# Optimization experiments

Measured on AMD Instinct MI355X. Metric: run time of the kernel, lower is better.

Reference implementation:

```python
import jax, jax.numpy as jnp
import numpy as np

N, E, IN, H, D, M, HID = 20000, 640000, 256, 8, 16, 3, 128


def setup_inputs() -> dict:
    key = jax.random.key(0)
    ks = jax.random.split(key, 9)
    h = jax.random.normal(ks[0], (N, IN), jnp.float32)
    # scale params for numerically sane attention logits
    fc_W = jax.random.normal(ks[1], (M, IN, H * D), jnp.float32) / np.sqrt(IN).astype(np.float32)
    attn_l = jax.random.normal(ks[2], (M, H, D), jnp.float32) * 0.1
    attn_r = jax.random.normal(ks[3], (M, H, D), jnp.float32) * 0.1
    bias = jnp.zeros((M, H * D), jnp.float32)
    edge_w = jax.random.uniform(ks[4], (M, E), jnp.float32)
    src = jax.random.randint(ks[5], (M, E), 0, N, jnp.int32)
    dst = jax.random.randint(ks[6], (M, E), 0, N, jnp.int32)
    sem_W1 = jax.random.normal(ks[7], (H * D, HID), jnp.float32) / np.sqrt(H * D).astype(np.float32)
    sem_b1 = jnp.zeros((HID,), jnp.float32)
    sem_w2 = jax.random.normal(ks[8], (HID,), jnp.float32) / np.sqrt(HID).astype(np.float32)
    return dict(h=h, fc_W=fc_W, attn_l=attn_l, attn_r=attn_r, bias=bias,
                edge_w=edge_w, sem_W1=sem_W1, sem_b1=sem_b1, sem_w2=sem_w2,
                src=src, dst=dst)


def _gat(h, W, al, ar, b, ew, s, d):
    # AdvGATConv forward, eval mode (dropout identity), residual=False
    ft = (h @ W).reshape(N, H, D)                      # [N,H,D]
    el = (ft * al).sum(-1)                             # [N,H]
    er = (ft * ar).sum(-1)                             # [N,H]
    # edge scores: (el_u + er_v) * edge_weight, then LeakyReLU(0.2)
    e = jax.nn.leaky_relu((el[s] + er[d]) * ew[:, None], 0.2)  # [E,H]
    # edge_softmax: segment softmax over incoming edges per dst node
    mx = jax.ops.segment_max(e, d, num_segments=N)
    mx = jnp.where(jnp.isfinite(mx), mx, 0.0)          # empty segments -> 0
    ex = jnp.exp(e - jax.lax.stop_gradient(mx)[d])
    denom = jax.ops.segment_sum(ex, d, num_segments=N)
    a = ex / denom[d]                                  # [E,H]
    # u_mul_e + sum: gather src feats, weight, scatter-add to dst
    out = jax.ops.segment_sum(ft[s] * a[:, :, None], d, num_segments=N)
    out = out + b.reshape(1, H, D)
    return jax.nn.elu(out).reshape(N, H * D)


def reference(h, fc_W, attn_l, attn_r, bias, edge_w, sem_W1, sem_b1, sem_w2, src, dst):
    embs = [_gat(h, fc_W[i], attn_l[i], attn_r[i], bias[i], edge_w[i], src[i], dst[i])
            for i in range(M)]
    z = jnp.stack(embs, axis=1)                        # [N, M, H*D]
    # SemanticAttention: mean over nodes of w2 . tanh(z W1 + b1), softmax over M
    w = (jnp.tanh(z @ sem_W1 + sem_b1) @ sem_w2).mean(0)  # [M]
    beta = jax.nn.softmax(w)
    return jnp.einsum('nmf,m->nf', z, beta)            # [N, H*D]
```

## Files before the change

### kernel.cpp

```cpp
#include <hip/hip_runtime.h>
#include <math.h>

#define NN 20000
#define NE 640000
#define NIN 256
#define NH 8
#define HD 16
#define NM 3
#define NF 128
#define HID 128
#define NSEG (NM * NN)
#define CAP 128

typedef __attribute__((ext_vector_type(4))) _Float16 half4;
typedef __attribute__((ext_vector_type(8))) _Float16 half8;
typedef __attribute__((ext_vector_type(4))) float f32x4;

__device__ __forceinline__ void atomAddF(float* p, float v) {
  unsafeAtomicAdd(p, v);
}

__global__ void k_prep(const float* __restrict__ h, const float* __restrict__ fcW,
                       const float* __restrict__ W1, _Float16* __restrict__ h16,
                       _Float16* __restrict__ WT, _Float16* __restrict__ W1T,
                       int* __restrict__ cursor, float* __restrict__ wsum) {
  int t = blockIdx.x * 256 + threadIdx.x;
  if (t < NN * NIN / 4) {
    float4 v = *(const float4*)(h + 4 * t);
    half4 o = {(_Float16)v.x, (_Float16)v.y, (_Float16)v.z, (_Float16)v.w};
    *(half4*)(h16 + 4 * t) = o;
  }
  if (t < NM * NIN * NF) {
    int mm = t >> 15;
    int n = (t >> 8) & 127;
    int k = t & 255;
    WT[t] = (_Float16)fcW[(mm << 15) + (k << 7) + n];
  }
  if (t < NF * HID) {
    int n = t >> 7;
    int k = t & 127;
    W1T[t] = (_Float16)W1[k * HID + n];
  }
  if (t < NSEG) cursor[t] = 0;
  if (t < 8) wsum[t] = 0.0f;
}

__device__ __forceinline__ void fill_body(int fb, const int* __restrict__ src,
                                          const int* __restrict__ dst,
                                          const float* __restrict__ ew,
                                          int* __restrict__ cursor,
                                          unsigned* __restrict__ erec) {
  int e4 = (fb * 256 + threadIdx.x) * 4;
  if (e4 >= NM * NE) return;
  int4 d4 = *(const int4*)(dst + e4);
  int4 s4 = *(const int4*)(src + e4);
  float4 w4 = *(const float4*)(ew + e4);
  const int dd[4] = {d4.x, d4.y, d4.z, d4.w};
  const int ss[4] = {s4.x, s4.y, s4.z, s4.w};
  const float ww[4] = {w4.x, w4.y, w4.z, w4.w};
  int seg[4], pos[4];
#pragma unroll
  for (int j = 0; j < 4; ++j) {
    int m = (e4 + j) / NE;
    seg[j] = m * NN + dd[j];
    pos[j] = atomicAdd(cursor + seg[j], 1);
  }
#pragma unroll
  for (int j = 0; j < 4; ++j) {
    unsigned wq = (unsigned)fminf(ww[j] * 131072.f, 131071.f);
    if (pos[j] < CAP)
      __builtin_nontemporal_store(((unsigned)ss[j] << 17) | wq,
                                  erec + (size_t)seg[j] * CAP + pos[j]);
  }
}

__device__ __forceinline__ void gemm_body(int g, const _Float16* __restrict__ h16,
                                          const _Float16* __restrict__ WT,
                                          const float* __restrict__ al,
                                          const float* __restrict__ ar,
                                          _Float16* __restrict__ fth,
                                          float* __restrict__ el,
                                          float* __restrict__ er) {
  int bx = g % 313, by = g / 313;
  int tid = threadIdx.x;
  int wave = tid >> 6, lane = tid & 63;
  int l15 = lane & 15, kslot = lane >> 4;
  int m = by >> 1;
  int cin = (by & 1) << 6;
  int rowbase = bx * 64 + wave * 16;
  int arow = rowbase + l15;
  bool aok = arow < NN;
  const _Float16* Ap = h16 + (size_t)(aok ? arow : 0) * NIN + kslot * 8;
  const _Float16* Bp = WT + ((size_t)m * NF + cin + l15) * NIN + kslot * 8;
  f32x4 acc[4];
#pragma unroll
  for (int c = 0; c < 4; ++c) acc[c] = (f32x4){0.f, 0.f, 0.f, 0.f};
#pragma unroll
  for (int kk = 0; kk < 8; ++kk) {
    int k0 = kk * 32;
    half8 a = {};
    if (aok) a = *(const half8*)(Ap + k0);
#pragma unroll
    for (int c = 0; c < 4; ++c) {
      half8 b = *(const half8*)(Bp + (size_t)c * 16 * NIN + k0);
      acc[c] = __builtin_amdgcn_mfma_f32_16x16x32_f16(a, b, acc[c], 0, 0, 0);
    }
  }
  int orow0 = rowbase + kslot * 4;
#pragma unroll
  for (int j = 0; j < 4; ++j) {
    int r = orow0 + j;
    if (r < NN) {
      _Float16* op = fth + ((size_t)m * NN + r) * NF + cin + l15;
#pragma unroll
      for (int c = 0; c < 4; ++c) op[c * 16] = (_Float16)acc[c][j];
    }
  }
  float alr[4], arr_[4];
#pragma unroll
  for (int c = 0; c < 4; ++c) {
    int head = (cin >> 4) + c;
    alr[c] = al[(m * NH + head) * HD + l15];
    arr_[c] = ar[(m * NH + head) * HD + l15];
  }
#pragma unroll
  for (int c = 0; c < 4; ++c) {
    int head = (cin >> 4) + c;
#pragma unroll
    for (int j = 0; j < 4; ++j) {
      float v = acc[c][j] * alr[c];
      float u = acc[c][j] * arr_[c];
#pragma unroll
      for (int off = 1; off < 16; off <<= 1) {
        v += __shfl_xor(v, off);
        u += __shfl_xor(u, off);
      }
      int r = orow0 + j;
      if (l15 == 0 && r < NN) {
        size_t idx = ((size_t)m * NN + r) * NH + head;
        el[idx] = v;
        er[idx] = u;
      }
    }
  }
}

__global__ __launch_bounds__(256) void k_fill_gemm(
    const int* __restrict__ src, const int* __restrict__ dst,
    const float* __restrict__ ew, int* __restrict__ cursor,
    unsigned* __restrict__ erec, const _Float16* __restrict__ h16,
    const _Float16* __restrict__ WT, const float* __restrict__ al,
    const float* __restrict__ ar, _Float16* __restrict__ fth,
    float* __restrict__ el, float* __restrict__ er) {
  int idx = blockIdx.x;
  int half_ = idx >> 1;
  if (idx & 1) {
    if (half_ < 1878) gemm_body(half_, h16, WT, al, ar, fth, el, er);
  } else {
    if (half_ < 1875) fill_body(half_, src, dst, ew, cursor, erec);
  }
}

__global__ __launch_bounds__(256) void k_aggr8(
    const int* __restrict__ cursor, const unsigned* __restrict__ erec,
    const float* __restrict__ el, const float* __restrict__ er,
    const _Float16* __restrict__ fth, const float* __restrict__ bias,
    _Float16* __restrict__ zh) {
  int wid = (blockIdx.x * 256 + threadIdx.x) >> 6;
  int lane = threadIdx.x & 63;
  if (wid >= NSEG) return;
  int m = wid / NN;
  int cnt = cursor[wid];
  cnt = cnt < CAP ? cnt : CAP;
  const unsigned* rp = erec + (size_t)wid * CAP;
  int g = lane >> 3, l8 = lane & 7;
  int h2 = l8;
  int c0 = l8 * 16;
  float er2 = er[wid * NH + h2];
  const float* elm = el + (size_t)m * NN * NH;
  const _Float16* fhm = fth + (size_t)m * NN * NF;

  float mx = -1e30f, sm = 0.f;
  float acc[16] = {};
  for (int i = g; i < cnt; i += 8) {
    unsigned rec = rp[i];
    int s = rec >> 17;
    float w = ((rec & 131071u) + 0.5f) * (1.f / 131072.f);
    float x = (elm[s * NH + h2] + er2) * w;
    x = x > 0.f ? x : 0.2f * x;
    float nmx = fmaxf(mx, x);
    float f = __expf(mx - nmx);
    float e = __expf(x - nmx);
    mx = nmx;
    sm = sm * f + e;
    const _Float16* fp = fhm + (size_t)s * NF + c0;
    half8 q0 = *(const half8*)(fp);
    half8 q1 = *(const half8*)(fp + 8);
#pragma unroll
    for (int k = 0; k < 8; ++k) acc[k] = fmaf(e, (float)q0[k], acc[k] * f);
#pragma unroll
    for (int k = 0; k < 8; ++k) acc[8 + k] = fmaf(e, (float)q1[k], acc[8 + k] * f);
  }
#pragma unroll
  for (int d = 8; d <= 32; d <<= 1) {
    float omx = __shfl_xor(mx, d);
    float osm = __shfl_xor(sm, d);
    float nmx = fmaxf(mx, omx);
    float f1 = __expf(mx - nmx), f2 = __expf(omx - nmx);
    sm = sm * f1 + osm * f2;
#pragma unroll
    for (int k = 0; k < 16; ++k) {
      float o = __shfl_xor(acc[k], d);
      acc[k] = acc[k] * f1 + o * f2;
    }
    mx = nmx;
  }
  if (g == 0) {
    float inv = sm > 0.f ? 1.f / sm : 0.f;
    const float* bp = bias + m * NF + c0;
    half8 zo0, zo1;
#pragma unroll
    for (int k = 0; k < 8; ++k) {
      float q = fmaf(acc[k], inv, bp[k]);
      q = q > 0.f ? q : __expf(q) - 1.f;
      zo0[k] = (_Float16)q;
      float q2 = fmaf(acc[8 + k], inv, bp[8 + k]);
      q2 = q2 > 0.f ? q2 : __expf(q2) - 1.f;
      zo1[k] = (_Float16)q2;
    }
    *(half8*)(zh + (size_t)wid * NF + c0) = zo0;
    *(half8*)(zh + (size_t)wid * NF + c0 + 8) = zo1;
  }
}

__global__ __launch_bounds__(256) void k_semgemm_mfma(
    const _Float16* __restrict__ zh, const _Float16* __restrict__ W1T,
    const float* __restrict__ b1, const float* __restrict__ w2,
    float* __restrict__ wsum) {
  __shared__ float msum[NM];
  int tid = threadIdx.x;
  if (tid < NM) msum[tid] = 0.f;
  __syncthreads();
  int wave = tid >> 6, lane = tid & 63;
  int l15 = lane & 15, kslot = lane >> 4;
  int rowbase = blockIdx.x * 64 + wave * 16;
  int arow = rowbase + l15;
  bool aok = arow < NSEG;
  const _Float16* Ap = zh + (size_t)(aok ? arow : 0) * NF + kslot * 8;
  const _Float16* Bp = W1T + (size_t)l15 * HID + kslot * 8;
  f32x4 acc[8];
#pragma unroll
  for (int c = 0; c < 8; ++c) acc[c] = (f32x4){0.f, 0.f, 0.f, 0.f};
#pragma unroll
  for (int kk = 0; kk < 4; ++kk) {
    int k0 = kk * 32;
    half8 a = {};
    if (aok) a = *(const half8*)(Ap + k0);
#pragma unroll
    for (int c = 0; c < 8; ++c) {
      half8 b = *(const half8*)(Bp + (size_t)c * 16 * HID + k0);
      acc[c] = __builtin_amdgcn_mfma_f32_16x16x32_f16(a, b, acc[c], 0, 0, 0);
    }
  }
  float p[4] = {0.f, 0.f, 0.f, 0.f};
#pragma unroll
  for (int c = 0; c < 8; ++c) {
    int col = c * 16 + l15;
    float b1r = b1[col];
    float w2r = w2[col];
#pragma unroll
    for (int j = 0; j < 4; ++j) p[j] += w2r * tanhf(acc[c][j] + b1r);
  }
#pragma unroll
  for (int j = 0; j < 4; ++j) {
#pragma unroll
    for (int off = 1; off < 16; off <<= 1) p[j] += __shfl_xor(p[j], off);
  }
  if (l15 == 0) {
#pragma unroll
    for (int j = 0; j < 4; ++j) {
      int r = rowbase + kslot * 4 + j;
      if (r < NSEG) atomicAdd(&msum[r / NN], p[j]);
    }
  }
  __syncthreads();
  if (tid < NM) {
    float v = msum[tid];
    if (v != 0.f) atomAddF(wsum + tid, v);
  }
}

__global__ void k_out8(const _Float16* __restrict__ zh, const float* __restrict__ wsum,
                       float* __restrict__ out) {
  int t = blockIdx.x * 256 + threadIdx.x;
  if (t >= NN * NF / 8) return;
  float w0 = wsum[0] * (1.f / NN);
  float w1 = wsum[1] * (1.f / NN);
  float w2v = wsum[2] * (1.f / NN);
  float mxw = fmaxf(w0, fmaxf(w1, w2v));
  float e0 = __expf(w0 - mxw), e1 = __expf(w1 - mxw), e2 = __expf(w2v - mxw);
  float inv = 1.f / (e0 + e1 + e2);
  e0 *= inv; e1 *= inv; e2 *= inv;
  size_t base = (size_t)t * 8;
  half8 z0 = *(const half8*)(zh + base);
  half8 z1 = *(const half8*)(zh + (size_t)NN * NF + base);
  half8 z2 = *(const half8*)(zh + (size_t)2 * NN * NF + base);
  float o[8];
#pragma unroll
  for (int k = 0; k < 8; ++k)
    o[k] = e0 * (float)z0[k] + e1 * (float)z1[k] + e2 * (float)z2[k];
  *(float4*)(out + base) = make_float4(o[0], o[1], o[2], o[3]);
  *(float4*)(out + base + 4) = make_float4(o[4], o[5], o[6], o[7]);
}

extern "C" void kernel_launch(void* const* d_in, const int* in_sizes, int n_in,
                              void* d_out, int out_size, void* d_ws, size_t ws_size,
                              hipStream_t stream) {
  (void)in_sizes; (void)n_in; (void)out_size; (void)ws_size;
  const float* h    = (const float*)d_in[0];
  const float* fcW  = (const float*)d_in[1];
  const float* al   = (const float*)d_in[2];
  const float* ar   = (const float*)d_in[3];
  const float* bias = (const float*)d_in[4];
  const float* ew   = (const float*)d_in[5];
  const float* W1   = (const float*)d_in[6];
  const float* b1   = (const float*)d_in[7];
  const float* w2   = (const float*)d_in[8];
  const int* src    = (const int*)d_in[9];
  const int* dst    = (const int*)d_in[10];
  float* out = (float*)d_out;

  char* base = (char*)d_ws;
  size_t o = 0;
  int* cursor = (int*)(base + o); o += (size_t)NSEG * 4;
  float* wsum = (float*)(base + o); o += 8 * 4;
  o = (o + 15) & ~(size_t)15;
  unsigned* erec = (unsigned*)(base + o); o += (size_t)NSEG * CAP * 4;
  float* el   = (float*)(base + o); o += (size_t)NSEG * NH * 4;
  float* er   = (float*)(base + o); o += (size_t)NSEG * NH * 4;
  _Float16* fth = (_Float16*)(base + o); o += (size_t)NM * NN * NF * 2;
  _Float16* h16 = (_Float16*)(base + o); o += (size_t)NN * NIN * 2;
  _Float16* WT  = (_Float16*)(base + o); o += (size_t)NM * NIN * NF * 2;
  _Float16* W1T = (_Float16*)(base + o); o += (size_t)NF * HID * 2;
  _Float16* zh  = (_Float16*)(base + o); o += (size_t)NM * NN * NF * 2;

  hipLaunchKernelGGL(k_prep, dim3(5000), dim3(256), 0, stream,
                     h, fcW, W1, h16, WT, W1T, cursor, wsum);
  hipLaunchKernelGGL(k_fill_gemm, dim3(3756), dim3(256), 0, stream,
                     src, dst, ew, cursor, erec, h16, WT, al, ar, fth, el, er);
  hipLaunchKernelGGL(k_aggr8, dim3(15000), dim3(256), 0, stream,
                     cursor, erec, el, er, fth, bias, zh);
  hipLaunchKernelGGL(k_semgemm_mfma, dim3(938), dim3(256), 0, stream,
                     zh, W1T, b1, w2, wsum);
  hipLaunchKernelGGL(k_out8, dim3(1250), dim3(256), 0, stream, zh, wsum, out);
}
```

Measured before the change: 215.2 us.

## Widen fill to 8 edges per thread, rebalance fused grid, split aggregation into halves

The fill stage now handles 8 edges per thread with nontemporal vector loads and computes the metapath index once per thread. The fused fill/GEMM grid is remapped so one fill block is interleaved with two GEMM blocks, giving 938 fill blocks and 1878 GEMM blocks. Aggregation launches twice as many waves, each handling half of the 128 feature columns. This cuts per-lane registers and raises occupancy, but every edge record, el value and exp computation is now repeated across the two passes.

```diff
diff --git a/kernel.cpp b/kernel.cpp
--- a/kernel.cpp
+++ b/kernel.cpp
@@ -15,6 +15,8 @@
 typedef __attribute__((ext_vector_type(4))) _Float16 half4;
 typedef __attribute__((ext_vector_type(8))) _Float16 half8;
 typedef __attribute__((ext_vector_type(4))) float f32x4;
+typedef __attribute__((ext_vector_type(4))) int i32x4;
+typedef __attribute__((ext_vector_type(4))) float f32x4v;
 
 __device__ __forceinline__ void atomAddF(float* p, float v) {
   unsafeAtomicAdd(p, v);
@@ -50,23 +52,26 @@
                                           const float* __restrict__ ew,
                                           int* __restrict__ cursor,
                                           unsigned* __restrict__ erec) {
-  int e4 = (fb * 256 + threadIdx.x) * 4;
-  if (e4 >= NM * NE) return;
-  int4 d4 = *(const int4*)(dst + e4);
-  int4 s4 = *(const int4*)(src + e4);
-  float4 w4 = *(const float4*)(ew + e4);
-  const int dd[4] = {d4.x, d4.y, d4.z, d4.w};
-  const int ss[4] = {s4.x, s4.y, s4.z, s4.w};
-  const float ww[4] = {w4.x, w4.y, w4.z, w4.w};
-  int seg[4], pos[4];
-#pragma unroll
-  for (int j = 0; j < 4; ++j) {
-    int m = (e4 + j) / NE;
+  int e8 = (fb * 256 + threadIdx.x) * 8;
+  if (e8 >= NM * NE) return;
+  i32x4 s0 = __builtin_nontemporal_load((const i32x4*)(src + e8));
+  i32x4 s1 = __builtin_nontemporal_load((const i32x4*)(src + e8 + 4));
+  i32x4 d0 = __builtin_nontemporal_load((const i32x4*)(dst + e8));
+  i32x4 d1 = __builtin_nontemporal_load((const i32x4*)(dst + e8 + 4));
+  f32x4v w0 = __builtin_nontemporal_load((const f32x4v*)(ew + e8));
+  f32x4v w1 = __builtin_nontemporal_load((const f32x4v*)(ew + e8 + 4));
+  const int ss[8] = {s0.x, s0.y, s0.z, s0.w, s1.x, s1.y, s1.z, s1.w};
+  const int dd[8] = {d0.x, d0.y, d0.z, d0.w, d1.x, d1.y, d1.z, d1.w};
+  const float ww[8] = {w0.x, w0.y, w0.z, w0.w, w1.x, w1.y, w1.z, w1.w};
+  int m = e8 / NE;
+  int seg[8], pos[8];
+#pragma unroll
+  for (int j = 0; j < 8; ++j) {
     seg[j] = m * NN + dd[j];
     pos[j] = atomicAdd(cursor + seg[j], 1);
   }
 #pragma unroll
-  for (int j = 0; j < 4; ++j) {
+  for (int j = 0; j < 8; ++j) {
     unsigned wq = (unsigned)fminf(ww[j] * 131072.f, 131071.f);
     if (pos[j] < CAP)
       __builtin_nontemporal_store(((unsigned)ss[j] << 17) | wq,
@@ -153,35 +158,39 @@
     const float* __restrict__ ar, _Float16* __restrict__ fth,
     float* __restrict__ el, float* __restrict__ er) {
   int idx = blockIdx.x;
-  int half_ = idx >> 1;
-  if (idx & 1) {
-    if (half_ < 1878) gemm_body(half_, h16, WT, al, ar, fth, el, er);
+  if (idx < 2814) {
+    int r = idx % 3;
+    int b = idx / 3;
+    if (r == 0) fill_body(b, src, dst, ew, cursor, erec);
+    else gemm_body(b * 2 + (r - 1), h16, WT, al, ar, fth, el, er);
   } else {
-    if (half_ < 1875) fill_body(half_, src, dst, ew, cursor, erec);
-  }
-}
-
-__global__ __launch_bounds__(256) void k_aggr8(
+    gemm_body(1876 + (idx - 2814), h16, WT, al, ar, fth, el, er);
+  }
+}
+
+__global__ __launch_bounds__(256) void k_aggr2p(
     const int* __restrict__ cursor, const unsigned* __restrict__ erec,
     const float* __restrict__ el, const float* __restrict__ er,
     const _Float16* __restrict__ fth, const float* __restrict__ bias,
     _Float16* __restrict__ zh) {
   int wid = (blockIdx.x * 256 + threadIdx.x) >> 6;
   int lane = threadIdx.x & 63;
-  if (wid >= NSEG) return;
-  int m = wid / NN;
-  int cnt = cursor[wid];
+  if (wid >= 2 * NSEG) return;
+  int pass = wid >= NSEG ? 1 : 0;
+  int seg = wid - pass * NSEG;
+  int m = seg / NN;
+  int cnt = cursor[seg];
   cnt = cnt < CAP ? cnt : CAP;
-  const unsigned* rp = erec + (size_t)wid * CAP;
+  const unsigned* rp = erec + (size_t)seg * CAP;
   int g = lane >> 3, l8 = lane & 7;
-  int h2 = l8;
-  int c0 = l8 * 16;
-  float er2 = er[wid * NH + h2];
+  int c0 = pass * 64 + l8 * 8;
+  int h2 = c0 >> 4;
+  float er2 = er[seg * NH + h2];
   const float* elm = el + (size_t)m * NN * NH;
   const _Float16* fhm = fth + (size_t)m * NN * NF;
 
   float mx = -1e30f, sm = 0.f;
-  float acc[16] = {};
+  float acc[8] = {};
   for (int i = g; i < cnt; i += 8) {
     unsigned rec = rp[i];
     int s = rec >> 17;
@@ -193,13 +202,9 @@
     float e = __expf(x - nmx);
     mx = nmx;
     sm = sm * f + e;
-    const _Float16* fp = fhm + (size_t)s * NF + c0;
-    half8 q0 = *(const half8*)(fp);
-    half8 q1 = *(const half8*)(fp + 8);
-#pragma unroll
-    for (int k = 0; k < 8; ++k) acc[k] = fmaf(e, (float)q0[k], acc[k] * f);
-#pragma unroll
-    for (int k = 0; k < 8; ++k) acc[8 + k] = fmaf(e, (float)q1[k], acc[8 + k] * f);
+    half8 q = *(const half8*)(fhm + (size_t)s * NF + c0);
+#pragma unroll
+    for (int k = 0; k < 8; ++k) acc[k] = fmaf(e, (float)q[k], acc[k] * f);
   }
 #pragma unroll
   for (int d = 8; d <= 32; d <<= 1) {
@@ -209,7 +214,7 @@
     float f1 = __expf(mx - nmx), f2 = __expf(omx - nmx);
     sm = sm * f1 + osm * f2;
 #pragma unroll
-    for (int k = 0; k < 16; ++k) {
+    for (int k = 0; k < 8; ++k) {
       float o = __shfl_xor(acc[k], d);
       acc[k] = acc[k] * f1 + o * f2;
     }
@@ -218,18 +223,14 @@
   if (g == 0) {
     float inv = sm > 0.f ? 1.f / sm : 0.f;
     const float* bp = bias + m * NF + c0;
-    half8 zo0, zo1;
+    half8 zo;
 #pragma unroll
     for (int k = 0; k < 8; ++k) {
       float q = fmaf(acc[k], inv, bp[k]);
       q = q > 0.f ? q : __expf(q) - 1.f;
-      zo0[k] = (_Float16)q;
-      float q2 = fmaf(acc[8 + k], inv, bp[8 + k]);
-      q2 = q2 > 0.f ? q2 : __expf(q2) - 1.f;
-      zo1[k] = (_Float16)q2;
-    }
-    *(half8*)(zh + (size_t)wid * NF + c0) = zo0;
-    *(half8*)(zh + (size_t)wid * NF + c0 + 8) = zo1;
+      zo[k] = (_Float16)q;
+    }
+    *(half8*)(zh + (size_t)seg * NF + c0) = zo;
   }
 }
 
@@ -346,9 +347,9 @@
 
   hipLaunchKernelGGL(k_prep, dim3(5000), dim3(256), 0, stream,
                      h, fcW, W1, h16, WT, W1T, cursor, wsum);
-  hipLaunchKernelGGL(k_fill_gemm, dim3(3756), dim3(256), 0, stream,
+  hipLaunchKernelGGL(k_fill_gemm, dim3(2816), dim3(256), 0, stream,
                      src, dst, ew, cursor, erec, h16, WT, al, ar, fth, el, er);
-  hipLaunchKernelGGL(k_aggr8, dim3(15000), dim3(256), 0, stream,
+  hipLaunchKernelGGL(k_aggr2p, dim3(30000), dim3(256), 0, stream,
                      cursor, erec, el, er, fth, bias, zh);
   hipLaunchKernelGGL(k_semgemm_mfma, dim3(938), dim3(256), 0, stream,
                      zh, W1T, b1, w2, wsum);
```

New measurement: 274.4 us. 27.5% more time.
